# Kernel tuning notes

Measured on AMD Instinct MI355X. Metric: run time of the kernel, lower is better.

## Reference

```python
import jax, jax.numpy as jnp
import numpy as np

LEAKY_SLOPE = 0.2  # DGL GATConv default negative_slope


def setup_inputs() -> dict:
    key = jax.random.key(0)
    ks = jax.random.split(key, 10)
    N_SRC, N_DST, E = 100000, 100000, 1600000
    H1, H0, D = 2, 2, 32          # in_h1_heads, in_h0_heads (GAT num_heads), out_dim
    IN1, IN0 = 128, 128           # in_h1_dim, in_h0_dim
    OUT_HEADS = 4
    return {
        "hier_1": jax.random.normal(ks[0], (N_SRC, H1, IN1), jnp.float32),
        "hier_0": jax.random.normal(ks[1], (N_DST, IN0), jnp.float32),
        "src_idx": jax.random.randint(ks[2], (E,), 0, N_SRC, jnp.int32),
        "dst_idx": jax.random.randint(ks[3], (E,), 0, N_DST, jnp.int32),
        "W_src": jax.random.normal(ks[4], (H0 * D, IN1), jnp.float32) * 0.05,
        "W_dst": jax.random.normal(ks[5], (H0 * D, IN0), jnp.float32) * 0.05,
        "attn_l": jax.random.normal(ks[6], (H0, D), jnp.float32) * 0.1,
        "attn_r": jax.random.normal(ks[7], (H0, D), jnp.float32) * 0.1,
        "gat_bias": jnp.zeros((H0, D), jnp.float32),
        "fc_W": jax.random.normal(ks[8], (OUT_HEADS, H1 * H0), jnp.float32),
        "fc_b": jnp.zeros((OUT_HEADS,), jnp.float32),
    }


def reference(hier_1, hier_0, src_idx, dst_idx, W_src, W_dst,
              attn_l, attn_r, gat_bias, fc_W, fc_b):
    N_src, H1, _ = hier_1.shape
    N_dst = hier_0.shape[0]
    H0, D = attn_l.shape

    # Shared GATConv projections (same weights reused across the H1 python loop
    # in the original -> vectorize over the H1 axis).
    feat_src = jnp.einsum('nhi,oi->nho', hier_1, W_src).reshape(N_src, H1, H0, D)
    feat_dst = (hier_0 @ W_dst.T).reshape(N_dst, H0, D)

    el = jnp.einsum('nhkd,kd->nhk', feat_src, attn_l)   # [N_src, H1, H0]
    er = jnp.einsum('nkd,kd->nk', feat_dst, attn_r)     # [N_dst, H0]

    # Edge attention logits + softmax over incoming edges per dst node.
    e = jax.nn.leaky_relu(el[src_idx] + er[dst_idx][:, None, :], LEAKY_SLOPE)  # [E,H1,H0]
    emax = jax.ops.segment_max(e, dst_idx, num_segments=N_dst)
    emax = jnp.where(jnp.isfinite(emax), emax, 0.0)     # zero-in-degree safety
    ee = jnp.exp(e - emax[dst_idx])
    denom = jax.ops.segment_sum(ee, dst_idx, num_segments=N_dst)
    alpha = ee / denom[dst_idx]                          # [E, H1, H0]

    # Aggregate messages: sum_e alpha * feat_src[src].
    msg = alpha[..., None] * feat_src[src_idx]           # [E, H1, H0, D]
    out = jax.ops.segment_sum(msg, dst_idx, num_segments=N_dst)  # [N_dst,H1,H0,D]
    out = out + gat_bias[None, None]                     # GATConv bias (per call)

    # cat over H1 (H1-major), transpose, softmax-normalized linear head mixing.
    res = out.reshape(N_dst, H1 * H0, D)
    res = jnp.swapaxes(res, 1, 2)                        # [N_dst, D, H1*H0]
    W = jax.nn.softmax(fc_W, axis=1)                     # normWeight: softmax(dim=1)
    res = res @ W.T + fc_b                               # [N_dst, D, out_heads]
    return jnp.swapaxes(res, 1, 2)                       # [N_dst, out_heads, D]
```

## Files before the change

kernel.cpp:

```cpp
#include <hip/hip_runtime.h>
#include <hip/hip_bf16.h>

typedef __attribute__((ext_vector_type(8))) short short8_t;
typedef __attribute__((ext_vector_type(4))) float float4v;

__device__ __forceinline__ float lrelu(float x) { return x > 0.f ? x : 0.2f * x; }
__device__ __forceinline__ float blo(unsigned u) { return __uint_as_float(u << 16); }
__device__ __forceinline__ float bhi(unsigned u) { return __uint_as_float(u & 0xffff0000u); }

__device__ __forceinline__ short8_t mk8(unsigned a, unsigned b, unsigned c, unsigned d) {
    union { unsigned u[4]; short8_t s; } x;
    x.u[0] = a; x.u[1] = b; x.u[2] = c; x.u[3] = d;
    return x.s;
}

__device__ __forceinline__ void split8(const float4& f0, const float4& f1,
                                       short8_t& hi8, short8_t& lo8) {
    float xs[8] = {f0.x, f0.y, f0.z, f0.w, f1.x, f1.y, f1.z, f1.w};
    unsigned h[4], l4[4];
#pragma unroll
    for (int p = 0; p < 4; ++p) {
        unsigned b0 = __float_as_uint(xs[2 * p]);
        unsigned b1 = __float_as_uint(xs[2 * p + 1]);
        unsigned h0b = b0 & 0xffff0000u, h1b = b1 & 0xffff0000u;
        h[p] = (h0b >> 16) | h1b;
        float l0 = xs[2 * p] - __uint_as_float(h0b);
        float l1 = xs[2 * p + 1] - __uint_as_float(h1b);
        l4[p] = (__float_as_uint(l0) >> 16) | (__float_as_uint(l1) & 0xffff0000u);
    }
    hi8 = mk8(h[0], h[1], h[2], h[3]);
    lo8 = mk8(l4[0], l4[1], l4[2], l4[3]);
}

__global__ void k_prep(const float* __restrict__ Wdst,
                       const float* __restrict__ attn_r,
                       const float* __restrict__ fcW,
                       const float* __restrict__ fcb,
                       const float* __restrict__ Wsrc,
                       float* __restrict__ w_er, float* __restrict__ Wn,
                       float* __restrict__ fb,
                       unsigned short* __restrict__ Wb_hi,
                       unsigned short* __restrict__ Wb_lo) {
    int t = threadIdx.x;
#pragma unroll
    for (int j = 0; j < 32; ++j) {
        int i = t + j * 256;
        float x = Wsrc[i];
        unsigned hb = __float_as_uint(x) & 0xffff0000u;
        float lf = x - __uint_as_float(hb);
        Wb_hi[i] = (unsigned short)(hb >> 16);
        Wb_lo[i] = (unsigned short)(__float_as_uint(lf) >> 16);
    }
    {
        int h0 = t >> 7, i = t & 127;
        float s = 0.f;
        for (int d = 0; d < 32; ++d)
            s += attn_r[h0 * 32 + d] * Wdst[(size_t)(h0 * 32 + d) * 128 + i];
        w_er[t] = s;
    }
    if (t < 16) {
        int oh = t >> 2, k = t & 3;
        float w[4], m = -1e30f;
        for (int j = 0; j < 4; ++j) {
            w[j] = fcW[oh * 4 + j];
            m = fmaxf(m, w[j]);
        }
        float s = 0.f;
        for (int j = 0; j < 4; ++j) s += __expf(w[j] - m);
        Wn[t] = __expf(w[k] - m) / s;
    }
    if (t < 4) fb[t] = fcb[t];
}

__global__ void k_hist(const int* __restrict__ dst, int* __restrict__ deg, int E) {
    int e = blockIdx.x * blockDim.x + threadIdx.x;
    if (e < E) atomicAdd(&deg[dst[e]], 1);
}

__global__ void k_alloc(const int* __restrict__ deg, int* __restrict__ off,
                        int* __restrict__ cursor, int* __restrict__ counter,
                        int N) {
    int d = blockIdx.x * blockDim.x + threadIdx.x;
    int lane = threadIdx.x & 63;
    int v = (d < N) ? deg[d] : 0;
    int inc = v;
#pragma unroll
    for (int m = 1; m < 64; m <<= 1) {
        int u = __shfl_up(inc, m, 64);
        if (lane >= m) inc += u;
    }
    int excl = inc - v;
    int base = 0;
    if (lane == 63) base = atomicAdd(counter, inc);
    base = __shfl(base, 63, 64);
    if (d < N) {
        off[d] = base + excl;
        cursor[d] = base + excl;
    }
}

__global__ __launch_bounds__(256) void k_featA(
        const float* __restrict__ hier1,
        const unsigned short* __restrict__ Wb_hi,
        const unsigned short* __restrict__ Wb_lo,
        const float* __restrict__ attn_l,
        const int* __restrict__ srcIdx, const int* __restrict__ dstIdx,
        int* __restrict__ cursor, int* __restrict__ ssrc,
        __hip_bfloat16* __restrict__ featb, float* __restrict__ el,
        int nrows, int E, int ntiles) {
    int t = threadIdx.x;
    int w = t >> 6, lane = t & 63;
    int lr = lane & 15;
    int lg = lane >> 4;

    int tile = blockIdx.x * 4 + w;
    bool hasTile = tile < ntiles;
    int m0 = tile * 16;

    float4 areg[8];
    if (hasTile) {
        int row_l = m0 + lr;
        if (row_l >= nrows) row_l = nrows - 1;
        const float* hrow = hier1 + (size_t)row_l * 128 + lg * 8;
#pragma unroll
        for (int kc = 0; kc < 4; ++kc) {
            areg[2 * kc]     = *reinterpret_cast<const float4*>(hrow + kc * 32);
            areg[2 * kc + 1] = *reinterpret_cast<const float4*>(hrow + kc * 32 + 4);
        }
    }

    for (int e = blockIdx.x * 256 + t; e < E; e += gridDim.x * 256) {
        int s = srcIdx[e];
        int d = dstIdx[e];
        int pos = atomicAdd(&cursor[d], 1);
        ssrc[pos] = s;
    }

    if (!hasTile) return;

    short8_t a_hi[4], a_lo[4];
#pragma unroll
    for (int kc = 0; kc < 4; ++kc)
        split8(areg[2 * kc], areg[2 * kc + 1], a_hi[kc], a_lo[kc]);

    float4v acc[4];
#pragma unroll
    for (int n = 0; n < 4; ++n) acc[n] = (float4v){0.f, 0.f, 0.f, 0.f};
#pragma unroll
    for (int n = 0; n < 4; ++n) {
        const unsigned short* bh = Wb_hi + (size_t)(n * 16 + lr) * 128 + lg * 8;
        const unsigned short* bl = Wb_lo + (size_t)(n * 16 + lr) * 128 + lg * 8;
#pragma unroll
        for (int kc = 0; kc < 4; ++kc) {
            short8_t Bh = *reinterpret_cast<const short8_t*>(bh + kc * 32);
            short8_t Bl = *reinterpret_cast<const short8_t*>(bl + kc * 32);
            acc[n] = __builtin_amdgcn_mfma_f32_16x16x32_bf16(a_lo[kc], Bh, acc[n], 0, 0, 0);
            acc[n] = __builtin_amdgcn_mfma_f32_16x16x32_bf16(a_hi[kc], Bl, acc[n], 0, 0, 0);
            acc[n] = __builtin_amdgcn_mfma_f32_16x16x32_bf16(a_hi[kc], Bh, acc[n], 0, 0, 0);
        }
    }

    float pe0[4] = {0.f, 0.f, 0.f, 0.f};
    float pe1[4] = {0.f, 0.f, 0.f, 0.f};
#pragma unroll
    for (int n = 0; n < 4; ++n) {
        float al = attn_l[n * 16 + lr];
#pragma unroll
        for (int r = 0; r < 4; ++r) {
            int row = m0 + lg * 4 + r;
            float v = acc[n][r];
            if (row < nrows)
                featb[((size_t)(row >> 1)) * 128 + (row & 1) * 64 + n * 16 + lr] =
                    __float2bfloat16(v);
            if (n < 2) pe0[r] += v * al; else pe1[r] += v * al;
        }
    }
#pragma unroll
    for (int m = 1; m <= 8; m <<= 1) {
#pragma unroll
        for (int r = 0; r < 4; ++r) {
            pe0[r] += __shfl_xor(pe0[r], m, 64);
            pe1[r] += __shfl_xor(pe1[r], m, 64);
        }
    }
    if (lr < 2) {
#pragma unroll
        for (int r = 0; r < 4; ++r) {
            int row = m0 + lg * 4 + r;
            float ev = lr ? pe1[r] : pe0[r];
            if (row < nrows) el[row * 2 + lr] = ev;
        }
    }
}

__global__ __launch_bounds__(256) void k_er(
        const float* __restrict__ hier0, const float* __restrict__ w_er,
        float* __restrict__ er, int Ndst, int ntilesE) {
    int t = threadIdx.x;
    int w = t >> 6, lane = t & 63;
    int lr = lane & 15, lg = lane >> 4;

    int tile = blockIdx.x * 4 + w;
    if (tile >= ntilesE) return;
    int m0 = tile * 16;

    short8_t Bh[4], Bl[4];
#pragma unroll
    for (int kc = 0; kc < 4; ++kc) {
        Bh[kc] = mk8(0, 0, 0, 0);
        Bl[kc] = mk8(0, 0, 0, 0);
    }
    if (lr < 2) {
#pragma unroll
        for (int kc = 0; kc < 4; ++kc) {
            float4 f0 = *reinterpret_cast<const float4*>(w_er + lr * 128 + kc * 32 + lg * 8);
            float4 f1 = *reinterpret_cast<const float4*>(w_er + lr * 128 + kc * 32 + lg * 8 + 4);
            split8(f0, f1, Bh[kc], Bl[kc]);
        }
    }

    int node = m0 + lr;
    if (node >= Ndst) node = Ndst - 1;
    const float* hrow = hier0 + (size_t)node * 128 + lg * 8;

    float4v acc = (float4v){0.f, 0.f, 0.f, 0.f};
#pragma unroll
    for (int kc = 0; kc < 4; ++kc) {
        float4 f0 = *reinterpret_cast<const float4*>(hrow + kc * 32);
        float4 f1 = *reinterpret_cast<const float4*>(hrow + kc * 32 + 4);
        short8_t a_hi, a_lo;
        split8(f0, f1, a_hi, a_lo);
        acc = __builtin_amdgcn_mfma_f32_16x16x32_bf16(a_lo, Bh[kc], acc, 0, 0, 0);
        acc = __builtin_amdgcn_mfma_f32_16x16x32_bf16(a_hi, Bl[kc], acc, 0, 0, 0);
        acc = __builtin_amdgcn_mfma_f32_16x16x32_bf16(a_hi, Bh[kc], acc, 0, 0, 0);
    }

    if (lr < 2) {
#pragma unroll
        for (int r = 0; r < 4; ++r) {
            int nn = m0 + lg * 4 + r;
            if (nn < Ndst) er[nn * 2 + lr] = acc[r];
        }
    }
}

__global__ __launch_bounds__(256) void k_gather(
        const int* __restrict__ ssrc, const int* __restrict__ off,
        const int* __restrict__ deg,
        const float* __restrict__ el, const float* __restrict__ er,
        const uint4* __restrict__ feat4,
        const float* __restrict__ bias,
        const float* __restrict__ Wn, const float* __restrict__ fb,
        float* __restrict__ out, int Ndst, int E) {
    __shared__ float g[4][128];
    int t = threadIdx.x;
    int wv = t >> 6, lane = t & 63;
    int d = blockIdx.x * 4 + wv;
    bool valid = d < Ndst;

    int q = lane >> 4;
    int c = lane & 15;
    int k = c >> 2;
    float erk = valid ? er[d * 2 + (k & 1)] : 0.f;
    int start = valid ? off[d] : 0;
    int n = valid ? deg[d] : 0;

    float a[8];
#pragma unroll
    for (int j = 0; j < 8; ++j) a[j] = 0.f;
    float den = 0.f;

    int base = start + q;
    int sA = ssrc[base < E ? base : 0];
    int sB = ssrc[(base + 4) < E ? (base + 4) : 0];
    uint4 fA = feat4[(size_t)sA * 16 + c];
    float eA = el[sA * 4 + k];

    for (int i = 0; i < n; i += 4) {
        uint4 fB = feat4[(size_t)sB * 16 + c];
        float eB = el[sB * 4 + k];
        int nx = base + i + 8;
        int sC = ssrc[nx < E ? nx : 0];

        bool ve = (i + q) < n;
        float ee = ve ? __expf(lrelu(eA + erk)) : 0.f;
        den += ee;
        a[0] = fmaf(ee, blo(fA.x), a[0]);
        a[1] = fmaf(ee, bhi(fA.x), a[1]);
        a[2] = fmaf(ee, blo(fA.y), a[2]);
        a[3] = fmaf(ee, bhi(fA.y), a[3]);
        a[4] = fmaf(ee, blo(fA.z), a[4]);
        a[5] = fmaf(ee, bhi(fA.z), a[5]);
        a[6] = fmaf(ee, blo(fA.w), a[6]);
        a[7] = fmaf(ee, bhi(fA.w), a[7]);

        sB = sC; fA = fB; eA = eB;
    }

#pragma unroll
    for (int m = 16; m <= 32; m <<= 1) {
        den += __shfl_xor(den, m, 64);
#pragma unroll
        for (int j = 0; j < 8; ++j) a[j] += __shfl_xor(a[j], m, 64);
    }

    float inv = den > 0.f ? 1.f / den : 0.f;
    if (q == 0) {
        int h0 = k & 1, ddb = (c & 3) * 8;
#pragma unroll
        for (int j = 0; j < 8; ++j)
            g[wv][c * 8 + j] = a[j] * inv + bias[h0 * 32 + ddb + j];
    }
    __syncthreads();

    if (valid) {
        int dd = (lane & 15) * 2;
        int oh = lane >> 4;
        float r0 = fb[oh], r1 = r0;
#pragma unroll
        for (int kk = 0; kk < 4; ++kk) {
            float wgt = Wn[oh * 4 + kk];
            r0 = fmaf(g[wv][kk * 32 + dd], wgt, r0);
            r1 = fmaf(g[wv][kk * 32 + dd + 1], wgt, r1);
        }
        *reinterpret_cast<float2*>(out + (size_t)d * 128 + lane * 2) =
            make_float2(r0, r1);
    }
}

extern "C" void kernel_launch(void* const* d_in, const int* in_sizes, int n_in,
                              void* d_out, int out_size, void* d_ws, size_t ws_size,
                              hipStream_t stream) {
    (void)n_in; (void)out_size; (void)ws_size;
    const float* hier1  = (const float*)d_in[0];
    const float* hier0  = (const float*)d_in[1];
    const int*   srcIdx = (const int*)d_in[2];
    const int*   dstIdx = (const int*)d_in[3];
    const float* Wsrc   = (const float*)d_in[4];
    const float* Wdst   = (const float*)d_in[5];
    const float* attn_l = (const float*)d_in[6];
    const float* attn_r = (const float*)d_in[7];
    const float* bias   = (const float*)d_in[8];
    const float* fcW    = (const float*)d_in[9];
    const float* fcb    = (const float*)d_in[10];
    float* out = (float*)d_out;

    const int Nsrc  = in_sizes[0] / 256;
    const int Ndst  = in_sizes[1] / 128;
    const int E     = in_sizes[2];
    const int nrows = Nsrc * 2;
    const int ntiles  = (nrows + 15) / 16;
    const int ntilesE = (Ndst + 15) / 16;

    __hip_bfloat16* featb = (__hip_bfloat16*)d_ws;
    unsigned short* Wb_hi = (unsigned short*)(featb + (size_t)Nsrc * 128);
    unsigned short* Wb_lo = Wb_hi + 8192;
    float* el   = (float*)(Wb_lo + 8192);
    float* er   = el   + (size_t)nrows * 2;
    float* w_er = er   + (size_t)Ndst * 2;
    float* Wn   = w_er + 256;
    float* fb   = Wn + 16;
    int*  deg     = (int*)(fb + 4);
    int*  off     = deg + Ndst;
    int*  cursor  = off + Ndst;
    int*  counter = cursor + Ndst;
    int*  ssrc    = counter + 1;

    hipMemsetAsync(deg, 0, (size_t)Ndst * sizeof(int), stream);
    hipMemsetAsync(counter, 0, sizeof(int), stream);

    k_prep<<<1, 256, 0, stream>>>(Wdst, attn_r, fcW, fcb, Wsrc,
                                  w_er, Wn, fb, Wb_hi, Wb_lo);

    k_hist<<<(E + 255) / 256, 256, 0, stream>>>(dstIdx, deg, E);

    k_alloc<<<(Ndst + 255) / 256, 256, 0, stream>>>(deg, off, cursor, counter, Ndst);

    int blocksA = (ntiles + 3) / 4;
    if (blocksA < 1) blocksA = 1;
    k_featA<<<blocksA, 256, 0, stream>>>(hier1, Wb_hi, Wb_lo, attn_l,
                                         srcIdx, dstIdx, cursor, ssrc,
                                         featb, el, nrows, E, ntiles);

    k_er<<<(ntilesE + 3) / 4, 256, 0, stream>>>(hier0, w_er, er, Ndst, ntilesE);

    k_gather<<<(Ndst + 3) / 4, 256, 0, stream>>>(ssrc, off, deg, el, er,
                                                 (const uint4*)featb,
                                                 bias, Wn, fb, out, Ndst, E);
}
```

Baseline: 486.8 us.

## Fuse er projection into featA, one edge per thread, widen gather lanes

Folds the k_er projection kernel into k_featA as extra wave tiles, dropping one launch. The edge-scatter loop becomes one edge per thread, with the grid sized to cover all edges. The edge loads are issued before the feature loads. In k_gather each lane now handles 16 features (two uint4 loads) and 8 edges run in parallel per wave instead of 4. This doubles the accumulator registers per lane and adds one more shuffle-reduction step.

Measured after the change: 462.5 us. 5.0% less time.

```diff
diff --git a/kernel.cpp b/kernel.cpp
--- a/kernel.cpp
+++ b/kernel.cpp
@@ -100,28 +100,41 @@
 }
 
 __global__ __launch_bounds__(256) void k_featA(
-        const float* __restrict__ hier1,
+        const float* __restrict__ hier1, const float* __restrict__ hier0,
         const unsigned short* __restrict__ Wb_hi,
         const unsigned short* __restrict__ Wb_lo,
-        const float* __restrict__ attn_l,
+        const float* __restrict__ attn_l, const float* __restrict__ w_er,
         const int* __restrict__ srcIdx, const int* __restrict__ dstIdx,
         int* __restrict__ cursor, int* __restrict__ ssrc,
         __hip_bfloat16* __restrict__ featb, float* __restrict__ el,
-        int nrows, int E, int ntiles) {
+        float* __restrict__ er,
+        int nrows, int Ndst, int E, int ntiles, int ntilesT) {
     int t = threadIdx.x;
     int w = t >> 6, lane = t & 63;
     int lr = lane & 15;
     int lg = lane >> 4;
 
+    int e = blockIdx.x * 256 + t;
+    bool hasE = e < E;
+    int es = 0, ed = 0;
+    if (hasE) { es = srcIdx[e]; ed = dstIdx[e]; }
+
     int tile = blockIdx.x * 4 + w;
-    bool hasTile = tile < ntiles;
-    int m0 = tile * 16;
+    bool isFeat = tile < ntiles;
+    bool isEr = (tile >= ntiles) && (tile < ntilesT);
 
     float4 areg[8];
-    if (hasTile) {
-        int row_l = m0 + lr;
-        if (row_l >= nrows) row_l = nrows - 1;
-        const float* hrow = hier1 + (size_t)row_l * 128 + lg * 8;
+    if (isFeat || isEr) {
+        const float* hrow;
+        if (isFeat) {
+            int row_l = tile * 16 + lr;
+            if (row_l >= nrows) row_l = nrows - 1;
+            hrow = hier1 + (size_t)row_l * 128 + lg * 8;
+        } else {
+            int node = (tile - ntiles) * 16 + lr;
+            if (node >= Ndst) node = Ndst - 1;
+            hrow = hier0 + (size_t)node * 128 + lg * 8;
+        }
 #pragma unroll
         for (int kc = 0; kc < 4; ++kc) {
             areg[2 * kc]     = *reinterpret_cast<const float4*>(hrow + kc * 32);
@@ -129,117 +142,97 @@
         }
     }
 
-    for (int e = blockIdx.x * 256 + t; e < E; e += gridDim.x * 256) {
-        int s = srcIdx[e];
-        int d = dstIdx[e];
-        int pos = atomicAdd(&cursor[d], 1);
-        ssrc[pos] = s;
-    }
-
-    if (!hasTile) return;
+    if (hasE) {
+        int pos = atomicAdd(&cursor[ed], 1);
+        ssrc[pos] = es;
+    }
+
+    if (!(isFeat || isEr)) return;
 
     short8_t a_hi[4], a_lo[4];
 #pragma unroll
     for (int kc = 0; kc < 4; ++kc)
         split8(areg[2 * kc], areg[2 * kc + 1], a_hi[kc], a_lo[kc]);
 
-    float4v acc[4];
-#pragma unroll
-    for (int n = 0; n < 4; ++n) acc[n] = (float4v){0.f, 0.f, 0.f, 0.f};
-#pragma unroll
-    for (int n = 0; n < 4; ++n) {
-        const unsigned short* bh = Wb_hi + (size_t)(n * 16 + lr) * 128 + lg * 8;
-        const unsigned short* bl = Wb_lo + (size_t)(n * 16 + lr) * 128 + lg * 8;
+    if (isFeat) {
+        int m0 = tile * 16;
+        float4v acc[4];
+#pragma unroll
+        for (int n = 0; n < 4; ++n) acc[n] = (float4v){0.f, 0.f, 0.f, 0.f};
+#pragma unroll
+        for (int n = 0; n < 4; ++n) {
+            const unsigned short* bh = Wb_hi + (size_t)(n * 16 + lr) * 128 + lg * 8;
+            const unsigned short* bl = Wb_lo + (size_t)(n * 16 + lr) * 128 + lg * 8;
+#pragma unroll
+            for (int kc = 0; kc < 4; ++kc) {
+                short8_t Bh = *reinterpret_cast<const short8_t*>(bh + kc * 32);
+                short8_t Bl = *reinterpret_cast<const short8_t*>(bl + kc * 32);
+                acc[n] = __builtin_amdgcn_mfma_f32_16x16x32_bf16(a_lo[kc], Bh, acc[n], 0, 0, 0);
+                acc[n] = __builtin_amdgcn_mfma_f32_16x16x32_bf16(a_hi[kc], Bl, acc[n], 0, 0, 0);
+                acc[n] = __builtin_amdgcn_mfma_f32_16x16x32_bf16(a_hi[kc], Bh, acc[n], 0, 0, 0);
+            }
+        }
+
+        float pe0[4] = {0.f, 0.f, 0.f, 0.f};
+        float pe1[4] = {0.f, 0.f, 0.f, 0.f};
+#pragma unroll
+        for (int n = 0; n < 4; ++n) {
+            float al = attn_l[n * 16 + lr];
+#pragma unroll
+            for (int r = 0; r < 4; ++r) {
+                int row = m0 + lg * 4 + r;
+                float v = acc[n][r];
+                if (row < nrows)
+                    featb[((size_t)(row >> 1)) * 128 + (row & 1) * 64 + n * 16 + lr] =
+                        __float2bfloat16(v);
+                if (n < 2) pe0[r] += v * al; else pe1[r] += v * al;
+            }
+        }
+#pragma unroll
+        for (int m = 1; m <= 8; m <<= 1) {
+#pragma unroll
+            for (int r = 0; r < 4; ++r) {
+                pe0[r] += __shfl_xor(pe0[r], m, 64);
+                pe1[r] += __shfl_xor(pe1[r], m, 64);
+            }
+        }
+        if (lr < 2) {
+#pragma unroll
+            for (int r = 0; r < 4; ++r) {
+                int row = m0 + lg * 4 + r;
+                float ev = lr ? pe1[r] : pe0[r];
+                if (row < nrows) el[row * 2 + lr] = ev;
+            }
+        }
+    } else {
+        int m0 = (tile - ntiles) * 16;
+        short8_t Bh[4], Bl[4];
 #pragma unroll
         for (int kc = 0; kc < 4; ++kc) {
-            short8_t Bh = *reinterpret_cast<const short8_t*>(bh + kc * 32);
-            short8_t Bl = *reinterpret_cast<const short8_t*>(bl + kc * 32);
-            acc[n] = __builtin_amdgcn_mfma_f32_16x16x32_bf16(a_lo[kc], Bh, acc[n], 0, 0, 0);
-            acc[n] = __builtin_amdgcn_mfma_f32_16x16x32_bf16(a_hi[kc], Bl, acc[n], 0, 0, 0);
-            acc[n] = __builtin_amdgcn_mfma_f32_16x16x32_bf16(a_hi[kc], Bh, acc[n], 0, 0, 0);
-        }
-    }
-
-    float pe0[4] = {0.f, 0.f, 0.f, 0.f};
-    float pe1[4] = {0.f, 0.f, 0.f, 0.f};
-#pragma unroll
-    for (int n = 0; n < 4; ++n) {
-        float al = attn_l[n * 16 + lr];
-#pragma unroll
-        for (int r = 0; r < 4; ++r) {
-            int row = m0 + lg * 4 + r;
-            float v = acc[n][r];
-            if (row < nrows)
-                featb[((size_t)(row >> 1)) * 128 + (row & 1) * 64 + n * 16 + lr] =
-                    __float2bfloat16(v);
-            if (n < 2) pe0[r] += v * al; else pe1[r] += v * al;
-        }
-    }
-#pragma unroll
-    for (int m = 1; m <= 8; m <<= 1) {
-#pragma unroll
-        for (int r = 0; r < 4; ++r) {
-            pe0[r] += __shfl_xor(pe0[r], m, 64);
-            pe1[r] += __shfl_xor(pe1[r], m, 64);
-        }
-    }
-    if (lr < 2) {
-#pragma unroll
-        for (int r = 0; r < 4; ++r) {
-            int row = m0 + lg * 4 + r;
-            float ev = lr ? pe1[r] : pe0[r];
-            if (row < nrows) el[row * 2 + lr] = ev;
-        }
-    }
-}
-
-__global__ __launch_bounds__(256) void k_er(
-        const float* __restrict__ hier0, const float* __restrict__ w_er,
-        float* __restrict__ er, int Ndst, int ntilesE) {
-    int t = threadIdx.x;
-    int w = t >> 6, lane = t & 63;
-    int lr = lane & 15, lg = lane >> 4;
-
-    int tile = blockIdx.x * 4 + w;
-    if (tile >= ntilesE) return;
-    int m0 = tile * 16;
-
-    short8_t Bh[4], Bl[4];
-#pragma unroll
-    for (int kc = 0; kc < 4; ++kc) {
-        Bh[kc] = mk8(0, 0, 0, 0);
-        Bl[kc] = mk8(0, 0, 0, 0);
-    }
-    if (lr < 2) {
+            Bh[kc] = mk8(0, 0, 0, 0);
+            Bl[kc] = mk8(0, 0, 0, 0);
+        }
+        if (lr < 2) {
+#pragma unroll
+            for (int kc = 0; kc < 4; ++kc) {
+                float4 f0 = *reinterpret_cast<const float4*>(w_er + lr * 128 + kc * 32 + lg * 8);
+                float4 f1 = *reinterpret_cast<const float4*>(w_er + lr * 128 + kc * 32 + lg * 8 + 4);
+                split8(f0, f1, Bh[kc], Bl[kc]);
+            }
+        }
+        float4v acc = (float4v){0.f, 0.f, 0.f, 0.f};
 #pragma unroll
         for (int kc = 0; kc < 4; ++kc) {
-            float4 f0 = *reinterpret_cast<const float4*>(w_er + lr * 128 + kc * 32 + lg * 8);
-            float4 f1 = *reinterpret_cast<const float4*>(w_er + lr * 128 + kc * 32 + lg * 8 + 4);
-            split8(f0, f1, Bh[kc], Bl[kc]);
-        }
-    }
-
-    int node = m0 + lr;
-    if (node >= Ndst) node = Ndst - 1;
-    const float* hrow = hier0 + (size_t)node * 128 + lg * 8;
-
-    float4v acc = (float4v){0.f, 0.f, 0.f, 0.f};
-#pragma unroll
-    for (int kc = 0; kc < 4; ++kc) {
-        float4 f0 = *reinterpret_cast<const float4*>(hrow + kc * 32);
-        float4 f1 = *reinterpret_cast<const float4*>(hrow + kc * 32 + 4);
-        short8_t a_hi, a_lo;
-        split8(f0, f1, a_hi, a_lo);
-        acc = __builtin_amdgcn_mfma_f32_16x16x32_bf16(a_lo, Bh[kc], acc, 0, 0, 0);
-        acc = __builtin_amdgcn_mfma_f32_16x16x32_bf16(a_hi, Bl[kc], acc, 0, 0, 0);
-        acc = __builtin_amdgcn_mfma_f32_16x16x32_bf16(a_hi, Bh[kc], acc, 0, 0, 0);
-    }
-
-    if (lr < 2) {
-#pragma unroll
-        for (int r = 0; r < 4; ++r) {
-            int nn = m0 + lg * 4 + r;
-            if (nn < Ndst) er[nn * 2 + lr] = acc[r];
+            acc = __builtin_amdgcn_mfma_f32_16x16x32_bf16(a_lo[kc], Bh[kc], acc, 0, 0, 0);
+            acc = __builtin_amdgcn_mfma_f32_16x16x32_bf16(a_hi[kc], Bl[kc], acc, 0, 0, 0);
+            acc = __builtin_amdgcn_mfma_f32_16x16x32_bf16(a_hi[kc], Bh[kc], acc, 0, 0, 0);
+        }
+        if (lr < 2) {
+#pragma unroll
+            for (int r = 0; r < 4; ++r) {
+                int nn = m0 + lg * 4 + r;
+                if (nn < Ndst) er[nn * 2 + lr] = acc[r];
+            }
         }
     }
 }
@@ -258,58 +251,69 @@
     int d = blockIdx.x * 4 + wv;
     bool valid = d < Ndst;
 
-    int q = lane >> 4;
-    int c = lane & 15;
-    int k = c >> 2;
+    int q = lane >> 3;
+    int c = lane & 7;
+    int k = c >> 1;
     float erk = valid ? er[d * 2 + (k & 1)] : 0.f;
     int start = valid ? off[d] : 0;
     int n = valid ? deg[d] : 0;
 
-    float a[8];
-#pragma unroll
-    for (int j = 0; j < 8; ++j) a[j] = 0.f;
+    float a[16];
+#pragma unroll
+    for (int j = 0; j < 16; ++j) a[j] = 0.f;
     float den = 0.f;
 
     int base = start + q;
     int sA = ssrc[base < E ? base : 0];
-    int sB = ssrc[(base + 4) < E ? (base + 4) : 0];
-    uint4 fA = feat4[(size_t)sA * 16 + c];
+    int sB = ssrc[(base + 8) < E ? (base + 8) : 0];
+    uint4 fA0 = feat4[(size_t)sA * 16 + 2 * c];
+    uint4 fA1 = feat4[(size_t)sA * 16 + 2 * c + 1];
     float eA = el[sA * 4 + k];
 
-    for (int i = 0; i < n; i += 4) {
-        uint4 fB = feat4[(size_t)sB * 16 + c];
+    for (int i = 0; i < n; i += 8) {
+        uint4 fB0 = feat4[(size_t)sB * 16 + 2 * c];
+        uint4 fB1 = feat4[(size_t)sB * 16 + 2 * c + 1];
         float eB = el[sB * 4 + k];
-        int nx = base + i + 8;
+        int nx = base + i + 16;
         int sC = ssrc[nx < E ? nx : 0];
 
         bool ve = (i + q) < n;
         float ee = ve ? __expf(lrelu(eA + erk)) : 0.f;
         den += ee;
-        a[0] = fmaf(ee, blo(fA.x), a[0]);
-        a[1] = fmaf(ee, bhi(fA.x), a[1]);
-        a[2] = fmaf(ee, blo(fA.y), a[2]);
-        a[3] = fmaf(ee, bhi(fA.y), a[3]);
-        a[4] = fmaf(ee, blo(fA.z), a[4]);
-        a[5] = fmaf(ee, bhi(fA.z), a[5]);
-        a[6] = fmaf(ee, blo(fA.w), a[6]);
-        a[7] = fmaf(ee, bhi(fA.w), a[7]);
-
-        sB = sC; fA = fB; eA = eB;
-    }
-
-#pragma unroll
-    for (int m = 16; m <= 32; m <<= 1) {
+        a[0]  = fmaf(ee, blo(fA0.x), a[0]);
+        a[1]  = fmaf(ee, bhi(fA0.x), a[1]);
+        a[2]  = fmaf(ee, blo(fA0.y), a[2]);
+        a[3]  = fmaf(ee, bhi(fA0.y), a[3]);
+        a[4]  = fmaf(ee, blo(fA0.z), a[4]);
+        a[5]  = fmaf(ee, bhi(fA0.z), a[5]);
+        a[6]  = fmaf(ee, blo(fA0.w), a[6]);
+        a[7]  = fmaf(ee, bhi(fA0.w), a[7]);
+        a[8]  = fmaf(ee, blo(fA1.x), a[8]);
+        a[9]  = fmaf(ee, bhi(fA1.x), a[9]);
+        a[10] = fmaf(ee, blo(fA1.y), a[10]);
+        a[11] = fmaf(ee, bhi(fA1.y), a[11]);
+        a[12] = fmaf(ee, blo(fA1.z), a[12]);
+        a[13] = fmaf(ee, bhi(fA1.z), a[13]);
+        a[14] = fmaf(ee, blo(fA1.w), a[14]);
+        a[15] = fmaf(ee, bhi(fA1.w), a[15]);
+
+        sB = sC; fA0 = fB0; fA1 = fB1; eA = eB;
+    }
+
+#pragma unroll
+    for (int m = 8; m <= 32; m <<= 1) {
         den += __shfl_xor(den, m, 64);
 #pragma unroll
-        for (int j = 0; j < 8; ++j) a[j] += __shfl_xor(a[j], m, 64);
+        for (int j = 0; j < 16; ++j) a[j] += __shfl_xor(a[j], m, 64);
     }
 
     float inv = den > 0.f ? 1.f / den : 0.f;
     if (q == 0) {
-        int h0 = k & 1, ddb = (c & 3) * 8;
-#pragma unroll
-        for (int j = 0; j < 8; ++j)
-            g[wv][c * 8 + j] = a[j] * inv + bias[h0 * 32 + ddb + j];
+        int h0 = k & 1;
+        int db = (c & 1) * 16;
+#pragma unroll
+        for (int j = 0; j < 16; ++j)
+            g[wv][c * 16 + j] = a[j] * inv + bias[h0 * 32 + db + j];
     }
     __syncthreads();
 
@@ -351,6 +355,7 @@
     const int nrows = Nsrc * 2;
     const int ntiles  = (nrows + 15) / 16;
     const int ntilesE = (Ndst + 15) / 16;
+    const int ntilesT = ntiles + ntilesE;
 
     __hip_bfloat16* featb = (__hip_bfloat16*)d_ws;
     unsigned short* Wb_hi = (unsigned short*)(featb + (size_t)Nsrc * 128);
@@ -376,13 +381,14 @@
 
     k_alloc<<<(Ndst + 255) / 256, 256, 0, stream>>>(deg, off, cursor, counter, Ndst);
 
-    int blocksA = (ntiles + 3) / 4;
-    if (blocksA < 1) blocksA = 1;
-    k_featA<<<blocksA, 256, 0, stream>>>(hier1, Wb_hi, Wb_lo, attn_l,
+    int blocksA = (ntilesT + 3) / 4;
+    int blocksE2 = (E + 255) / 256;
+    if (blocksE2 > blocksA) blocksA = blocksE2;
+    k_featA<<<blocksA, 256, 0, stream>>>(hier1, hier0, Wb_hi, Wb_lo,
+                                         attn_l, w_er,
                                          srcIdx, dstIdx, cursor, ssrc,
-                                         featb, el, nrows, E, ntiles);
-
-    k_er<<<(ntilesE + 3) / 4, 256, 0, stream>>>(hier0, w_er, er, Ndst, ntilesE);
+                                         featb, el, er,
+                                         nrows, Ndst, E, ntiles, ntilesT);
 
     k_gather<<<(Ndst + 3) / 4, 256, 0, stream>>>(ssrc, off, deg, el, er,
                                                  (const uint4*)featb,
```
